# Kernel optimization log

Measured on AMD Instinct MI355X. Metric: run time of the kernel, lower is better.

The kernel has to match this reference:

```python
import jax, jax.numpy as jnp
import numpy as np

EMBED_DIM = 1024
NUM_HEADS = 16
NUM_KV_HEADS = 4
HEAD_DIM = 64
GQA_RATIO = NUM_HEADS // NUM_KV_HEADS
SCALE = 1.0 / np.sqrt(HEAD_DIM).astype(np.float32)
B, L = 1, 4096
NUM_SEQS = 8  # 8 packed sequences of length 512


def setup_inputs() -> dict:
    key = jax.random.key(0)
    k1, k2, k3, k4, k5 = jax.random.split(key, 5)
    hidden_states = jax.random.normal(k1, (B, L, EMBED_DIM), dtype=jnp.float32)
    cu_seqlens = (jnp.arange(NUM_SEQS + 1, dtype=jnp.int32) * (L // NUM_SEQS))
    s = 1.0 / np.sqrt(EMBED_DIM)
    Wq = jax.random.normal(k2, (EMBED_DIM, NUM_HEADS * HEAD_DIM), dtype=jnp.float32) * s
    Wk = jax.random.normal(k3, (EMBED_DIM, NUM_KV_HEADS * HEAD_DIM), dtype=jnp.float32) * s
    Wv = jax.random.normal(k4, (EMBED_DIM, NUM_KV_HEADS * HEAD_DIM), dtype=jnp.float32) * s
    Wo = jax.random.normal(k5, (NUM_HEADS * HEAD_DIM, EMBED_DIM), dtype=jnp.float32) * s
    return {"hidden_states": hidden_states, "Wq": Wq, "Wk": Wk, "Wv": Wv, "Wo": Wo,
            "cu_seqlens": cu_seqlens}


def reference(hidden_states, Wq, Wk, Wv, Wo, cu_seqlens):
    b, l, d = hidden_states.shape
    # QKV projections (Linear, no bias)
    q = (hidden_states @ Wq).reshape(b, l, NUM_HEADS, HEAD_DIM)
    k = (hidden_states @ Wk).reshape(b, l, NUM_KV_HEADS, HEAD_DIM)
    v = (hidden_states @ Wv).reshape(b, l, NUM_KV_HEADS, HEAD_DIM)
    # GQA: expand kv heads to num_heads (faithful to module's manual expand)
    k = jnp.repeat(k, GQA_RATIO, axis=2)  # [b, l, H, hd]
    v = jnp.repeat(v, GQA_RATIO, axis=2)
    # [b, H, l, hd]
    q = q.transpose(0, 2, 1, 3)
    k = k.transpose(0, 2, 1, 3)
    v = v.transpose(0, 2, 1, 3)
    # block-diagonal varlen mask from cu_seqlens
    pos = jnp.arange(l, dtype=jnp.int32)
    seq_ids = jnp.searchsorted(cu_seqlens, pos, side='right') - 1  # [l]
    mask = seq_ids[:, None] == seq_ids[None, :]                    # [l, l]
    # dense SDPA with mask
    scores = jnp.einsum('bhqd,bhkd->bhqk', q, k) * SCALE
    scores = jnp.where(mask[None, None], scores, jnp.finfo(scores.dtype).min)
    attn = jax.nn.softmax(scores, axis=-1)
    out = jnp.einsum('bhqk,bhkd->bhqd', attn, v)
    out = out.transpose(0, 2, 1, 3).reshape(b, l, NUM_HEADS * HEAD_DIM)
    return out @ Wo
```

## Files before the change

### kernel.cpp

```cpp
#include <hip/hip_runtime.h>
#include <hip/hip_bf16.h>
#include <stdint.h>
#include <stddef.h>

typedef __attribute__((ext_vector_type(8))) short short8;
typedef __attribute__((ext_vector_type(4))) short short4v;
typedef __attribute__((ext_vector_type(4))) float f32x4;

__device__ inline void store_c(float* p, float v) { *p = v; }
__device__ inline void store_c(__hip_bfloat16* p, float v) { *p = __float2bfloat16(v); }

__global__ __launch_bounds__(256) void convert_kernel(const float* __restrict__ in,
                                                      __hip_bfloat16* __restrict__ out,
                                                      int n4)
{
    int i = blockIdx.x * blockDim.x + threadIdx.x;
    if (i >= n4) return;
    const f32x4 v = *(const f32x4*)(in + (size_t)i * 4);
    union { __hip_bfloat16 t[4]; short4v s4; } u;
    #pragma unroll
    for (int j = 0; j < 4; ++j) u.t[j] = __float2bfloat16(v[j]);
    *(short4v*)(out + (size_t)i * 4) = u.s4;
}

__global__ __launch_bounds__(256) void transpose_kernel(const float* __restrict__ Wq,
                                                        const float* __restrict__ Wk,
                                                        const float* __restrict__ Wv,
                                                        const float* __restrict__ Wo,
                                                        __hip_bfloat16* __restrict__ Wt)
{
    __shared__ float tile[32][33];
    const int bk = blockIdx.x;
    const int bn = blockIdx.y;
    const int tx = threadIdx.x & 31;
    const int ty = threadIdx.x >> 5;
    const int n0 = bn * 32;

    const float* src; int ld; int col0;
    if (n0 < 1024)      { src = Wq; ld = 1024; col0 = n0; }
    else if (n0 < 1280) { src = Wk; ld = 256;  col0 = n0 - 1024; }
    else if (n0 < 1536) { src = Wv; ld = 256;  col0 = n0 - 1280; }
    else                { src = Wo; ld = 1024; col0 = n0 - 1536; }

    #pragma unroll
    for (int r = 0; r < 4; ++r) {
        int k = ty + 8 * r;
        tile[k][tx] = src[(size_t)(bk * 32 + k) * ld + col0 + tx];
    }
    __syncthreads();
    #pragma unroll
    for (int r = 0; r < 4; ++r) {
        int nl = ty + 8 * r;
        Wt[(size_t)(n0 + nl) * 1024 + bk * 32 + tx] = __float2bfloat16(tile[tx][nl]);
    }
}

#define GBM 128
#define GBN 128
#define GBK 32
#define GLDK 40

template <typename CT>
__global__ __launch_bounds__(256) void gemm_bt_kernel(const __hip_bfloat16* __restrict__ A,
                                                      const __hip_bfloat16* __restrict__ Bt,
                                                      CT* __restrict__ C,
                                                      int M, int N, int K)
{
    __shared__ __align__(16) __hip_bfloat16 As[GBM][GLDK];
    __shared__ __align__(16) __hip_bfloat16 Bs[GBN][GLDK];

    const int tid  = threadIdx.x;
    const int lane = tid & 63;
    const int wave = tid >> 6;
    const int wm = wave >> 1;
    const int wn = wave & 1;
    const int bm = blockIdx.x;
    const int bn = blockIdx.y;

    const int fr = lane & 15;
    const int fk = (lane >> 4) * 8;

    const size_t arow0 = (size_t)bm * GBM;
    const size_t brow0 = (size_t)bn * GBN;

    f32x4 acc[4][4];
    const f32x4 z4 = {0.f, 0.f, 0.f, 0.f};
    #pragma unroll
    for (int i = 0; i < 4; ++i)
        #pragma unroll
        for (int j = 0; j < 4; ++j) acc[i][j] = z4;

    short8 ra[2], rb[2];
    #pragma unroll
    for (int i = 0; i < 2; ++i) {
        int c = tid + 256 * i;
        int r = c >> 2, ko = (c & 3) * 8;
        ra[i] = *(const short8*)(A  + (arow0 + r) * K + ko);
        rb[i] = *(const short8*)(Bt + (brow0 + r) * K + ko);
    }

    for (int k0 = 0; k0 < K; k0 += GBK) {
        #pragma unroll
        for (int i = 0; i < 2; ++i) {
            int c = tid + 256 * i;
            int r = c >> 2, ko = (c & 3) * 8;
            *(short8*)&As[r][ko] = ra[i];
            *(short8*)&Bs[r][ko] = rb[i];
        }
        __syncthreads();
        if (k0 + GBK < K) {
            int k1 = k0 + GBK;
            #pragma unroll
            for (int i = 0; i < 2; ++i) {
                int c = tid + 256 * i;
                int r = c >> 2, ko = (c & 3) * 8;
                ra[i] = *(const short8*)(A  + (arow0 + r) * K + k1 + ko);
                rb[i] = *(const short8*)(Bt + (brow0 + r) * K + k1 + ko);
            }
        }
        short8 af[4], bfv[4];
        #pragma unroll
        for (int mf = 0; mf < 4; ++mf)
            af[mf] = *(const short8*)&As[wm * 64 + mf * 16 + fr][fk];
        #pragma unroll
        for (int nf = 0; nf < 4; ++nf)
            bfv[nf] = *(const short8*)&Bs[wn * 64 + nf * 16 + fr][fk];
        #pragma unroll
        for (int mf = 0; mf < 4; ++mf)
            #pragma unroll
            for (int nf = 0; nf < 4; ++nf)
                acc[mf][nf] = __builtin_amdgcn_mfma_f32_16x16x32_bf16(af[mf], bfv[nf], acc[mf][nf], 0, 0, 0);
        __syncthreads();
    }

    const int crow = bm * GBM + wm * 64;
    const int ccol = bn * GBN + wn * 64;
    #pragma unroll
    for (int mf = 0; mf < 4; ++mf)
        #pragma unroll
        for (int nf = 0; nf < 4; ++nf)
            #pragma unroll
            for (int r = 0; r < 4; ++r) {
                int row = crow + mf * 16 + (lane >> 4) * 4 + r;
                int col = ccol + nf * 16 + fr;
                store_c(&C[(size_t)row * N + col], acc[mf][nf][r]);
            }
}

__global__ __launch_bounds__(256) void attn_kernel(const __hip_bfloat16* __restrict__ QKV,
                                                   __hip_bfloat16* __restrict__ O)
{
    __shared__ __align__(16) __hip_bfloat16 Ks[64][72];
    __shared__ __align__(16) __hip_bfloat16 Vts[64][72];
    __shared__ __align__(16) __hip_bfloat16 Ps[4][32][72];

    const int tid  = threadIdx.x;
    const int lane = tid & 63;
    const int wave = tid >> 6;
    const int qt = blockIdx.x;
    const int h  = blockIdx.y;
    const int sq = blockIdx.z;
    const int kvh = h >> 2;

    const int fr = lane & 15;
    const int fg = lane >> 4;
    const int fk = fg * 8;

    const int q0 = sq * 512 + qt * 128 + wave * 32;

    short8 qf[2][2];
    #pragma unroll
    for (int mf = 0; mf < 2; ++mf)
        #pragma unroll
        for (int kc = 0; kc < 2; ++kc)
            qf[mf][kc] = *(const short8*)(QKV + (size_t)(q0 + mf * 16 + fr) * 1536 + h * 64 + kc * 32 + fk);

    const f32x4 z4 = {0.f, 0.f, 0.f, 0.f};
    f32x4 acc_o[2][4];
    #pragma unroll
    for (int a = 0; a < 2; ++a)
        #pragma unroll
        for (int b = 0; b < 4; ++b) acc_o[a][b] = z4;

    float m_run[2][4], l_run[2][4];
    #pragma unroll
    for (int a = 0; a < 2; ++a)
        #pragma unroll
        for (int r = 0; r < 4; ++r) { m_run[a][r] = -1e30f; l_run[a][r] = 0.f; }

    const float cs = 0.125f * 1.44269504088896340736f;

    for (int t = 0; t < 8; ++t) {
        const int kvbase = sq * 512 + t * 64;

        #pragma unroll
        for (int i = 0; i < 2; ++i) {
            int cc = tid + 256 * i;
            int r = cc >> 3, dch = cc & 7;
            short8 v = *(const short8*)(QKV + (size_t)(kvbase + r) * 1536 + 1024 + kvh * 64 + dch * 8);
            *(short8*)&Ks[r][dch * 8] = v;
        }
        #pragma unroll
        for (int i = 0; i < 2; ++i) {
            int kv = tid & 63;
            int dc = (tid >> 6) + 4 * i;
            short8 v = *(const short8*)(QKV + (size_t)(kvbase + kv) * 1536 + 1280 + kvh * 64 + dc * 8);
            #pragma unroll
            for (int b = 0; b < 8; ++b)
                Vts[dc * 8 + b][kv] = ((const __hip_bfloat16*)&v)[b];
        }
        __syncthreads();

        f32x4 s[2][4];
        #pragma unroll
        for (int a = 0; a < 2; ++a)
            #pragma unroll
            for (int b = 0; b < 4; ++b) s[a][b] = z4;
        #pragma unroll
        for (int nf = 0; nf < 4; ++nf) {
            short8 kf0 = *(const short8*)&Ks[nf * 16 + fr][fk];
            short8 kf1 = *(const short8*)&Ks[nf * 16 + fr][32 + fk];
            #pragma unroll
            for (int mf = 0; mf < 2; ++mf) {
                s[mf][nf] = __builtin_amdgcn_mfma_f32_16x16x32_bf16(qf[mf][0], kf0, s[mf][nf], 0, 0, 0);
                s[mf][nf] = __builtin_amdgcn_mfma_f32_16x16x32_bf16(qf[mf][1], kf1, s[mf][nf], 0, 0, 0);
            }
        }

        #pragma unroll
        for (int mf = 0; mf < 2; ++mf) {
            #pragma unroll
            for (int r = 0; r < 4; ++r) {
                float mx = fmaxf(fmaxf(s[mf][0][r], s[mf][1][r]), fmaxf(s[mf][2][r], s[mf][3][r]));
                #pragma unroll
                for (int off = 1; off < 16; off <<= 1)
                    mx = fmaxf(mx, __shfl_xor(mx, off));
                float mnew = fmaxf(m_run[mf][r], mx);
                float f = exp2f((m_run[mf][r] - mnew) * cs);
                m_run[mf][r] = mnew;
                float p0 = exp2f((s[mf][0][r] - mnew) * cs);
                float p1 = exp2f((s[mf][1][r] - mnew) * cs);
                float p2 = exp2f((s[mf][2][r] - mnew) * cs);
                float p3 = exp2f((s[mf][3][r] - mnew) * cs);
                l_run[mf][r] = l_run[mf][r] * f + (p0 + p1 + p2 + p3);
                #pragma unroll
                for (int nf = 0; nf < 4; ++nf)
                    acc_o[mf][nf][r] *= f;
                int rl = mf * 16 + fg * 4 + r;
                Ps[wave][rl][ 0 + fr] = __float2bfloat16(p0);
                Ps[wave][rl][16 + fr] = __float2bfloat16(p1);
                Ps[wave][rl][32 + fr] = __float2bfloat16(p2);
                Ps[wave][rl][48 + fr] = __float2bfloat16(p3);
            }
        }

        #pragma unroll
        for (int kc = 0; kc < 2; ++kc) {
            short8 pa[2];
            #pragma unroll
            for (int mf = 0; mf < 2; ++mf)
                pa[mf] = *(const short8*)&Ps[wave][mf * 16 + fr][kc * 32 + fk];
            #pragma unroll
            for (int nf = 0; nf < 4; ++nf) {
                short8 vf = *(const short8*)&Vts[nf * 16 + fr][kc * 32 + fk];
                #pragma unroll
                for (int mf = 0; mf < 2; ++mf)
                    acc_o[mf][nf] = __builtin_amdgcn_mfma_f32_16x16x32_bf16(pa[mf], vf, acc_o[mf][nf], 0, 0, 0);
            }
        }
        __syncthreads();
    }

    #pragma unroll
    for (int mf = 0; mf < 2; ++mf) {
        #pragma unroll
        for (int r = 0; r < 4; ++r) {
            float lsum = l_run[mf][r];
            #pragma unroll
            for (int off = 1; off < 16; off <<= 1)
                lsum += __shfl_xor(lsum, off);
            float inv_l = 1.0f / lsum;
            int row = q0 + mf * 16 + fg * 4 + r;
            #pragma unroll
            for (int nf = 0; nf < 4; ++nf)
                O[(size_t)row * 1024 + h * 64 + nf * 16 + fr] =
                    __float2bfloat16(acc_o[mf][nf][r] * inv_l);
        }
    }
}

extern "C" void kernel_launch(void* const* d_in, const int* in_sizes, int n_in,
                              void* d_out, int out_size, void* d_ws, size_t ws_size,
                              hipStream_t stream)
{
    const float* hs = (const float*)d_in[0];
    const float* Wq = (const float*)d_in[1];
    const float* Wk = (const float*)d_in[2];
    const float* Wv = (const float*)d_in[3];
    const float* Wo = (const float*)d_in[4];

    char* ws = (char*)d_ws;
    __hip_bfloat16* hsb  = (__hip_bfloat16*)(ws);
    __hip_bfloat16* Wt   = (__hip_bfloat16*)(ws + 8388608);
    __hip_bfloat16* QKV  = (__hip_bfloat16*)(ws + 13631488);
    __hip_bfloat16* AOut = (__hip_bfloat16*)(ws + 26214400);
    float* out = (float*)d_out;

    convert_kernel<<<4096, 256, 0, stream>>>(hs, hsb, 1048576);
    transpose_kernel<<<dim3(32, 80), 256, 0, stream>>>(Wq, Wk, Wv, Wo, Wt);
    gemm_bt_kernel<__hip_bfloat16><<<dim3(32, 12), 256, 0, stream>>>(hsb, Wt, QKV, 4096, 1536, 1024);
    attn_kernel<<<dim3(4, 16, 8), 256, 0, stream>>>(QKV, AOut);
    gemm_bt_kernel<float><<<dim3(32, 8), 256, 0, stream>>>(AOut, Wt + (size_t)1536 * 1024, out, 4096, 1024, 1024);
}
```

Baseline: 168.1 us.

## Use direct global-to-LDS loads in GEMMs, smaller tiles, and vectorized P stores

Both projection GEMMs switch to a templated kernel that loads tiles straight from global memory into LDS with the global_load_lds builtin. This drops the register staging and the explicit prefetch, and the tiles shrink to 64x128 so more blocks launch. In attention, the P tile is written as one 4-element vector per row, and V-transpose columns are permuted to match, so the writes touch fewer LDS locations. The cost is losing the software prefetch overlap and using an unpadded LDS layout, which may bring bank conflicts.

```diff
diff --git a/kernel.cpp b/kernel.cpp
--- a/kernel.cpp
+++ b/kernel.cpp
@@ -9,6 +9,18 @@
 
 __device__ inline void store_c(float* p, float v) { *p = v; }
 __device__ inline void store_c(__hip_bfloat16* p, float v) { *p = __float2bfloat16(v); }
+
+__device__ __forceinline__ void gld_lds16(const __hip_bfloat16* g, __hip_bfloat16* l)
+{
+#if __has_builtin(__builtin_amdgcn_global_load_lds)
+    __builtin_amdgcn_global_load_lds(
+        (const __attribute__((address_space(1))) unsigned int*)g,
+        (__attribute__((address_space(3))) unsigned int*)l,
+        16, 0, 0);
+#else
+    *(short8*)((char*)l + (threadIdx.x & 63) * 16) = *(const short8*)g;
+#endif
+}
 
 __global__ __launch_bounds__(256) void convert_kernel(const float* __restrict__ in,
                                                       __hip_bfloat16* __restrict__ out,
@@ -55,90 +67,68 @@
     }
 }
 
-#define GBM 128
-#define GBN 128
-#define GBK 32
-#define GLDK 40
-
-template <typename CT>
-__global__ __launch_bounds__(256) void gemm_bt_kernel(const __hip_bfloat16* __restrict__ A,
-                                                      const __hip_bfloat16* __restrict__ Bt,
-                                                      CT* __restrict__ C,
-                                                      int M, int N, int K)
-{
-    __shared__ __align__(16) __hip_bfloat16 As[GBM][GLDK];
-    __shared__ __align__(16) __hip_bfloat16 Bs[GBN][GLDK];
+#define BK 32
+
+template <int BM, int BN, typename CT>
+__global__ __launch_bounds__(256) void gemm_gld_kernel(const __hip_bfloat16* __restrict__ A,
+                                                       const __hip_bfloat16* __restrict__ Bt,
+                                                       CT* __restrict__ C,
+                                                       int M, int N, int K)
+{
+    constexpr int MF = BM / 32;
+    constexpr int NF = BN / 32;
+    __shared__ __align__(16) __hip_bfloat16 As[BM * BK];
+    __shared__ __align__(16) __hip_bfloat16 Bs[BN * BK];
 
     const int tid  = threadIdx.x;
     const int lane = tid & 63;
     const int wave = tid >> 6;
     const int wm = wave >> 1;
     const int wn = wave & 1;
-    const int bm = blockIdx.x;
-    const int bn = blockIdx.y;
-
     const int fr = lane & 15;
     const int fk = (lane >> 4) * 8;
 
-    const size_t arow0 = (size_t)bm * GBM;
-    const size_t brow0 = (size_t)bn * GBN;
-
-    f32x4 acc[4][4];
+    const __hip_bfloat16* Ab = A  + (size_t)(blockIdx.x * BM) * K;
+    const __hip_bfloat16* Bb = Bt + (size_t)(blockIdx.y * BN) * K;
+
+    const int srow = lane >> 2;
+    const int scol = (lane & 3) * 8;
+
+    f32x4 acc[MF][NF];
     const f32x4 z4 = {0.f, 0.f, 0.f, 0.f};
     #pragma unroll
-    for (int i = 0; i < 4; ++i)
-        #pragma unroll
-        for (int j = 0; j < 4; ++j) acc[i][j] = z4;
-
-    short8 ra[2], rb[2];
-    #pragma unroll
-    for (int i = 0; i < 2; ++i) {
-        int c = tid + 256 * i;
-        int r = c >> 2, ko = (c & 3) * 8;
-        ra[i] = *(const short8*)(A  + (arow0 + r) * K + ko);
-        rb[i] = *(const short8*)(Bt + (brow0 + r) * K + ko);
-    }
-
-    for (int k0 = 0; k0 < K; k0 += GBK) {
-        #pragma unroll
-        for (int i = 0; i < 2; ++i) {
-            int c = tid + 256 * i;
-            int r = c >> 2, ko = (c & 3) * 8;
-            *(short8*)&As[r][ko] = ra[i];
-            *(short8*)&Bs[r][ko] = rb[i];
-        }
+    for (int i = 0; i < MF; ++i)
+        #pragma unroll
+        for (int j = 0; j < NF; ++j) acc[i][j] = z4;
+
+    for (int k0 = 0; k0 < K; k0 += BK) {
+        for (int i = wave; i < BM / 16; i += 4)
+            gld_lds16(Ab + (size_t)(i * 16 + srow) * K + k0 + scol, &As[i * 512]);
+        for (int i = wave; i < BN / 16; i += 4)
+            gld_lds16(Bb + (size_t)(i * 16 + srow) * K + k0 + scol, &Bs[i * 512]);
         __syncthreads();
-        if (k0 + GBK < K) {
-            int k1 = k0 + GBK;
-            #pragma unroll
-            for (int i = 0; i < 2; ++i) {
-                int c = tid + 256 * i;
-                int r = c >> 2, ko = (c & 3) * 8;
-                ra[i] = *(const short8*)(A  + (arow0 + r) * K + k1 + ko);
-                rb[i] = *(const short8*)(Bt + (brow0 + r) * K + k1 + ko);
-            }
-        }
-        short8 af[4], bfv[4];
-        #pragma unroll
-        for (int mf = 0; mf < 4; ++mf)
-            af[mf] = *(const short8*)&As[wm * 64 + mf * 16 + fr][fk];
-        #pragma unroll
-        for (int nf = 0; nf < 4; ++nf)
-            bfv[nf] = *(const short8*)&Bs[wn * 64 + nf * 16 + fr][fk];
-        #pragma unroll
-        for (int mf = 0; mf < 4; ++mf)
-            #pragma unroll
-            for (int nf = 0; nf < 4; ++nf)
+
+        short8 af[MF], bfv[NF];
+        #pragma unroll
+        for (int mf = 0; mf < MF; ++mf)
+            af[mf] = *(const short8*)&As[(wm * (BM / 2) + mf * 16 + fr) * BK + fk];
+        #pragma unroll
+        for (int nf = 0; nf < NF; ++nf)
+            bfv[nf] = *(const short8*)&Bs[(wn * (BN / 2) + nf * 16 + fr) * BK + fk];
+        #pragma unroll
+        for (int mf = 0; mf < MF; ++mf)
+            #pragma unroll
+            for (int nf = 0; nf < NF; ++nf)
                 acc[mf][nf] = __builtin_amdgcn_mfma_f32_16x16x32_bf16(af[mf], bfv[nf], acc[mf][nf], 0, 0, 0);
         __syncthreads();
     }
 
-    const int crow = bm * GBM + wm * 64;
-    const int ccol = bn * GBN + wn * 64;
-    #pragma unroll
-    for (int mf = 0; mf < 4; ++mf)
-        #pragma unroll
-        for (int nf = 0; nf < 4; ++nf)
+    const int crow = blockIdx.x * BM + wm * (BM / 2);
+    const int ccol = blockIdx.y * BN + wn * (BN / 2);
+    #pragma unroll
+    for (int mf = 0; mf < MF; ++mf)
+        #pragma unroll
+        for (int nf = 0; nf < NF; ++nf)
             #pragma unroll
             for (int r = 0; r < 4; ++r) {
                 int row = crow + mf * 16 + (lane >> 4) * 4 + r;
@@ -200,14 +190,17 @@
             short8 v = *(const short8*)(QKV + (size_t)(kvbase + r) * 1536 + 1024 + kvh * 64 + dch * 8);
             *(short8*)&Ks[r][dch * 8] = v;
         }
-        #pragma unroll
-        for (int i = 0; i < 2; ++i) {
-            int kv = tid & 63;
-            int dc = (tid >> 6) + 4 * i;
-            short8 v = *(const short8*)(QKV + (size_t)(kvbase + kv) * 1536 + 1280 + kvh * 64 + dc * 8);
-            #pragma unroll
-            for (int b = 0; b < 8; ++b)
-                Vts[dc * 8 + b][kv] = ((const __hip_bfloat16*)&v)[b];
+        {
+            const int kv = tid & 63;
+            const int pos = (kv & 15) * 4 + (kv >> 4);
+            #pragma unroll
+            for (int i = 0; i < 2; ++i) {
+                int dc = (tid >> 6) + 4 * i;
+                short8 v = *(const short8*)(QKV + (size_t)(kvbase + kv) * 1536 + 1280 + kvh * 64 + dc * 8);
+                #pragma unroll
+                for (int b = 0; b < 8; ++b)
+                    Vts[dc * 8 + b][pos] = ((const __hip_bfloat16*)&v)[b];
+            }
         }
         __syncthreads();
 
@@ -247,10 +240,12 @@
                 for (int nf = 0; nf < 4; ++nf)
                     acc_o[mf][nf][r] *= f;
                 int rl = mf * 16 + fg * 4 + r;
-                Ps[wave][rl][ 0 + fr] = __float2bfloat16(p0);
-                Ps[wave][rl][16 + fr] = __float2bfloat16(p1);
-                Ps[wave][rl][32 + fr] = __float2bfloat16(p2);
-                Ps[wave][rl][48 + fr] = __float2bfloat16(p3);
+                union { __hip_bfloat16 h[4]; short4v s4; } pw;
+                pw.h[0] = __float2bfloat16(p0);
+                pw.h[1] = __float2bfloat16(p1);
+                pw.h[2] = __float2bfloat16(p2);
+                pw.h[3] = __float2bfloat16(p3);
+                *(short4v*)&Ps[wave][rl][fr * 4] = pw.s4;
             }
         }
 
@@ -308,7 +303,7 @@
 
     convert_kernel<<<4096, 256, 0, stream>>>(hs, hsb, 1048576);
     transpose_kernel<<<dim3(32, 80), 256, 0, stream>>>(Wq, Wk, Wv, Wo, Wt);
-    gemm_bt_kernel<__hip_bfloat16><<<dim3(32, 12), 256, 0, stream>>>(hsb, Wt, QKV, 4096, 1536, 1024);
+    gemm_gld_kernel<64, 128, __hip_bfloat16><<<dim3(64, 12), 256, 0, stream>>>(hsb, Wt, QKV, 4096, 1536, 1024);
     attn_kernel<<<dim3(4, 16, 8), 256, 0, stream>>>(QKV, AOut);
-    gemm_bt_kernel<float><<<dim3(32, 8), 256, 0, stream>>>(AOut, Wt + (size_t)1536 * 1024, out, 4096, 1024, 1024);
-}
+    gemm_gld_kernel<64, 128, float><<<dim3(64, 8), 256, 0, stream>>>(AOut, Wt + (size_t)1536 * 1024, out, 4096, 1024, 1024);
+}
```

After: 167.3 us. About the same (-0.5%).
